# Kernel tuning notes

Hardware: AMD Instinct MI355X
Metric: run time of the kernel (lower is better)

Reference implementation:

```python
import jax, jax.numpy as jnp
import numpy as np

N = 100000   # nodes
E = 1000000  # edges
DIN = 128    # atom_in_features
DE = 16      # edge_attr_dim
H = 128      # hidden width (preprocess/cheb/postprocess)
K = 3        # Chebyshev order
EPS = 1e-5


def setup_inputs() -> dict:
    key = jax.random.key(0)
    ks = jax.random.split(key, 16)
    s = 0.02
    return {
        "x": jax.random.normal(ks[0], (N, DIN), jnp.float32),
        "edge_index": jax.random.randint(ks[1], (2, E), 0, N),
        "edge_attr": jax.random.normal(ks[2], (E, DE), jnp.float32),
        # AtomEdgeInteraction linear: (DIN+DE) -> H
        "w_int": jax.random.normal(ks[3], (DIN + DE, H), jnp.float32) * s,
        "b_int": jnp.zeros((H,), jnp.float32),
        # preprocess layer 1: Linear + BatchNorm + ReLU
        "w_pre": jax.random.normal(ks[4], (H, H), jnp.float32) * s,
        "b_pre": jnp.zeros((H,), jnp.float32),
        "g_pre": jnp.ones((H,), jnp.float32),
        "be_pre": jnp.zeros((H,), jnp.float32),
        # ChebConv layers: weight [K, in, out] + bias
        "cheb1_w": jax.random.normal(ks[5], (K, H, H), jnp.float32) * s,
        "cheb1_b": jnp.zeros((H,), jnp.float32),
        "cheb2_w": jax.random.normal(ks[6], (K, H, H), jnp.float32) * s,
        "cheb2_b": jnp.zeros((H,), jnp.float32),
        # postprocess: Linear + BatchNorm + ReLU
        "w_post": jax.random.normal(ks[7], (H, H), jnp.float32) * s,
        "b_post": jnp.zeros((H,), jnp.float32),
        "g_post": jnp.ones((H,), jnp.float32),
        "be_post": jnp.zeros((H,), jnp.float32),
        # output layer H -> 1
        "w_out": jax.random.normal(ks[8], (H, 1), jnp.float32) * s,
        "b_out": jnp.zeros((1,), jnp.float32),
    }


def _bn(z, g, b):
    # BatchNorm1d, training-mode batch statistics (biased variance, like torch)
    m = z.mean(0)
    v = ((z - m) ** 2).mean(0)
    return g * (z - m) * jax.lax.rsqrt(v + EPS) + b


def _cheb(h, W, b, row, col, norm):
    # ChebConv with sym normalization, lambda_max=2 => L_hat = -D^{-1/2} A D^{-1/2}
    def lhat(z):
        return jax.ops.segment_sum(norm[:, None] * z[row], col, num_segments=N)

    Tx0 = h
    out = Tx0 @ W[0]
    Tx1 = lhat(Tx0)
    out = out + Tx1 @ W[1]
    for k in range(2, W.shape[0]):
        Tx2 = 2.0 * lhat(Tx1) - Tx0
        out = out + Tx2 @ W[k]
        Tx0, Tx1 = Tx1, Tx2
    return out + b


def reference(x, edge_index, edge_attr,
              w_int, b_int,
              w_pre, b_pre, g_pre, be_pre,
              cheb1_w, cheb1_b, cheb2_w, cheb2_b,
              w_post, b_post, g_post, be_post,
              w_out, b_out):
    row, col = edge_index[0], edge_index[1]
    ones_e = jnp.ones((E,), x.dtype)

    # AtomEdgeInteraction: gather -> concat -> linear -> scatter_mean over col
    comb = jnp.concatenate([x[row], edge_attr], axis=-1)  # [E, DIN+DE]
    upd = comb @ w_int + b_int                             # [E, H]
    cnt = jax.ops.segment_sum(ones_e, col, num_segments=N)
    h = jax.ops.segment_sum(upd, col, num_segments=N) / jnp.clip(cnt, 1.0)[:, None]

    # preprocess layer 1 (Linear + BN + ReLU; dropout rate 0)
    h = jax.nn.relu(_bn(h @ w_pre + b_pre, g_pre, be_pre))

    # sym-normalized edge coefficients for scaled Laplacian
    deg = jax.ops.segment_sum(ones_e, row, num_segments=N)
    dis = jnp.where(deg > 0, jax.lax.rsqrt(jnp.maximum(deg, 1.0)), 0.0)
    norm = -dis[row] * dis[col]  # [E]

    h = jax.nn.relu(_cheb(h, cheb1_w, cheb1_b, row, col, norm))
    h = jax.nn.relu(_cheb(h, cheb2_w, cheb2_b, row, col, norm))

    # postprocess (Linear + BN + ReLU)
    h = jax.nn.relu(_bn(h @ w_post + b_post, g_post, be_post))

    # output layer, squeeze(-1) -> [N]
    return (h @ w_out + b_out).squeeze(-1)
```

## Files before the change

### kernel.cpp

```cpp
#include <hip/hip_runtime.h>
#include <hip/hip_bf16.h>

using u16 = unsigned short;
using u32 = unsigned int;

#define NN 100000
#define NE 1000000

typedef __attribute__((ext_vector_type(8))) short bfrag;
typedef __attribute__((ext_vector_type(4))) float ffrag;

__device__ __forceinline__ float bf2f(u16 u) { return __uint_as_float(((u32)u) << 16); }
__device__ __forceinline__ u16 f2bf(float f) {
  u32 x = __float_as_uint(f);
  return (u16)((x + 0x7fffu + ((x >> 16) & 1u)) >> 16);
}
__device__ __forceinline__ float rdv(const void* p, long i, int f) {
  return f ? bf2f(((const u16*)p)[i]) : ((const float*)p)[i];
}
__device__ __forceinline__ void acc8(float* a, uint4 v, float w) {
  a[0] = fmaf(w, __uint_as_float(v.x << 16), a[0]);
  a[1] = fmaf(w, __uint_as_float(v.x & 0xffff0000u), a[1]);
  a[2] = fmaf(w, __uint_as_float(v.y << 16), a[2]);
  a[3] = fmaf(w, __uint_as_float(v.y & 0xffff0000u), a[3]);
  a[4] = fmaf(w, __uint_as_float(v.z << 16), a[4]);
  a[5] = fmaf(w, __uint_as_float(v.z & 0xffff0000u), a[5]);
  a[6] = fmaf(w, __uint_as_float(v.w << 16), a[6]);
  a[7] = fmaf(w, __uint_as_float(v.w & 0xffff0000u), a[7]);
}

__global__ void k_flag(const u32* __restrict__ g_pre_raw, int* flag) {
  if (threadIdx.x == 0) flag[0] = (g_pre_raw[0] == 0x3F803F80u) ? 1 : 0;
}

#define OWXT 0
#define OWPRE 16384
#define OWD1 32768
#define OW11 49152
#define OV21 65536
#define OWD2 81920
#define OW12 98304
#define OV22 114688
#define OWPOST 131072
#define OWET 147456

struct PrepArgs { const void* in[16]; };

__global__ void k_prep(PrepArgs a, const int* __restrict__ flag, u16* __restrict__ wq,
                       float* __restrict__ wf) {
  int t = blockIdx.x * 256 + threadIdx.x;
  int f = *flag;
  if (t < 16384) {
    int o = t >> 7, k = t & 127;
    int ko = k * 128 + o;
    int ok = o * 128 + k;
    wq[OWXT + ok] = f2bf(rdv(a.in[0], ko, f));
    wq[OWPRE + ok] = f2bf(rdv(a.in[2], ko, f));
    float c0 = rdv(a.in[6], ko, f);
    float c1 = rdv(a.in[6], 16384 + ko, f);
    float c2 = rdv(a.in[6], 32768 + ko, f);
    wq[OWD1 + ok] = f2bf(c0 - c2);
    wq[OW11 + ok] = f2bf(c1);
    wq[OV21 + ok] = f2bf(2.f * c2);
    float d0 = rdv(a.in[8], ko, f);
    float d1 = rdv(a.in[8], 16384 + ko, f);
    float d2 = rdv(a.in[8], 32768 + ko, f);
    wq[OWD2 + ok] = f2bf(d0 - d2);
    wq[OW12 + ok] = f2bf(d1);
    wq[OV22 + ok] = f2bf(2.f * d2);
    wq[OWPOST + ok] = f2bf(rdv(a.in[10], ko, f));
  }
  if (t < 4096) {
    int o = t >> 5, k = t & 31;
    wq[OWET + o * 32 + k] = (k < 16) ? f2bf(rdv(a.in[0], (long)(128 + k) * 128 + o, f)) : (u16)0;
  }
  if (t < 1281) {
    int s = t >> 7, j = t & 127;
    const int map[11] = {1, 3, 4, 5, 7, 9, 11, 12, 13, 14, 15};
    wf[t] = rdv(a.in[map[s]], j, f);
  }
}

__global__ void k_hist(const int* __restrict__ ei, int* cnt, int* deg) {
  int e = blockIdx.x * 256 + threadIdx.x;
  if (e >= NE) return;
  atomicAdd(&deg[ei[e]], 1);
  atomicAdd(&cnt[ei[NE + e]], 1);
}

__global__ void k_scan1(const int* __restrict__ cnt, int* off, int* bsum) {
  __shared__ int s[1024];
  int t = threadIdx.x;
  int g = blockIdx.x * 1024 + t;
  int v = (g < NN) ? cnt[g] : 0;
  s[t] = v;
  __syncthreads();
  for (int st = 1; st < 1024; st <<= 1) {
    int x = (t >= st) ? s[t - st] : 0;
    __syncthreads();
    s[t] += x;
    __syncthreads();
  }
  if (g < NN) off[g] = s[t] - v;
  if (t == 1023) bsum[blockIdx.x] = s[t];
}

__global__ void k_scan2(int* bsum, int nb) {
  __shared__ int s[128];
  int t = threadIdx.x;
  int v = (t < nb) ? bsum[t] : 0;
  s[t] = v;
  __syncthreads();
  for (int st = 1; st < 128; st <<= 1) {
    int x = (t >= st) ? s[t - st] : 0;
    __syncthreads();
    s[t] += x;
    __syncthreads();
  }
  if (t < nb) bsum[t] = s[t] - v;
}

__global__ void k_scan3(int* off, const int* __restrict__ bsum,
                        const int* __restrict__ deg, float* __restrict__ dis) {
  int g = blockIdx.x * 1024 + threadIdx.x;
  if (g < NN) {
    off[g] += bsum[blockIdx.x];
    int d = deg[g];
    dis[g] = d > 0 ? rsqrtf((float)d) : 0.f;
  }
  if (g == 0) off[NN] = NE;
}

__global__ void k_place(const int* __restrict__ ei, const int* __restrict__ off,
                        int* cur, int* crow, int* ceid) {
  int e = blockIdx.x * 256 + threadIdx.x;
  if (e >= NE) return;
  int r = ei[e], c = ei[NE + e];
  int p = off[c] + atomicAdd(&cur[c], 1);
  crow[p] = r;
  ceid[p] = e;
}

__global__ __launch_bounds__(256) void k_spmm(const u16* __restrict__ src,
                                              u16* __restrict__ dst,
                                              const int* __restrict__ off,
                                              const int* __restrict__ crow,
                                              const float* __restrict__ dis,
                                              const u16* __restrict__ G, int relu) {
  int t = threadIdx.x;
  int node = blockIdx.x * 8 + (t >> 5);
  if (node >= NN) return;
  int l = t & 31;
  int half = l >> 4;
  int c = (l & 15) * 8;
  int p0 = off[node], p1 = off[node + 1];
  float a[8];
#pragma unroll
  for (int j = 0; j < 8; j++) a[j] = 0.f;
  const u16* sp = src + c;
  if (dis) {
    float nc = -dis[node];
    int p = p0 + half;
    for (; p + 6 < p1; p += 8) {
      int r0 = crow[p], r1 = crow[p + 2], r2 = crow[p + 4], r3 = crow[p + 6];
      float w0 = nc * dis[r0], w1 = nc * dis[r1];
      float w2 = nc * dis[r2], w3 = nc * dis[r3];
      uint4 v0 = *(const uint4*)(sp + (long)r0 * 128);
      uint4 v1 = *(const uint4*)(sp + (long)r1 * 128);
      uint4 v2 = *(const uint4*)(sp + (long)r2 * 128);
      uint4 v3 = *(const uint4*)(sp + (long)r3 * 128);
      acc8(a, v0, w0);
      acc8(a, v1, w1);
      acc8(a, v2, w2);
      acc8(a, v3, w3);
    }
    for (; p < p1; p += 2) {
      int r = crow[p];
      acc8(a, *(const uint4*)(sp + (long)r * 128), nc * dis[r]);
    }
  } else {
    int p = p0 + half;
    for (; p + 6 < p1; p += 8) {
      int r0 = crow[p], r1 = crow[p + 2], r2 = crow[p + 4], r3 = crow[p + 6];
      uint4 v0 = *(const uint4*)(sp + (long)r0 * 128);
      uint4 v1 = *(const uint4*)(sp + (long)r1 * 128);
      uint4 v2 = *(const uint4*)(sp + (long)r2 * 128);
      uint4 v3 = *(const uint4*)(sp + (long)r3 * 128);
      acc8(a, v0, 1.f);
      acc8(a, v1, 1.f);
      acc8(a, v2, 1.f);
      acc8(a, v3, 1.f);
    }
    for (; p < p1; p += 2) acc8(a, *(const uint4*)(sp + (long)crow[p] * 128), 1.f);
  }
#pragma unroll
  for (int j = 0; j < 8; j++) a[j] += __shfl_xor(a[j], 16);
  if (half) return;
  if (G) acc8(a, *(const uint4*)(G + (long)node * 128 + c), 1.f);
  if (relu) {
#pragma unroll
    for (int j = 0; j < 8; j++) a[j] = fmaxf(a[j], 0.f);
  }
  uint4 o;
  o.x = (u32)f2bf(a[0]) | ((u32)f2bf(a[1]) << 16);
  o.y = (u32)f2bf(a[2]) | ((u32)f2bf(a[3]) << 16);
  o.z = (u32)f2bf(a[4]) | ((u32)f2bf(a[5]) << 16);
  o.w = (u32)f2bf(a[6]) | ((u32)f2bf(a[7]) << 16);
  *(uint4*)(dst + (long)node * 128 + c) = o;
}

__global__ __launch_bounds__(256) void k_asum(const void* __restrict__ eattr,
                                              const int* __restrict__ flag,
                                              u16* __restrict__ asum,
                                              const int* __restrict__ off,
                                              const int* __restrict__ ceid) {
  int t = blockIdx.x * 256 + threadIdx.x;
  int node = t >> 4;
  if (node >= NN) return;
  int j = t & 15;
  int p0 = off[node], p1 = off[node + 1];
  float a = 0.f;
  if (*flag) {
    const u16* e16 = (const u16*)eattr;
    int p = p0;
    for (; p + 4 <= p1; p += 4) {
      float v0 = bf2f(e16[(long)ceid[p] * 16 + j]);
      float v1 = bf2f(e16[(long)ceid[p + 1] * 16 + j]);
      float v2 = bf2f(e16[(long)ceid[p + 2] * 16 + j]);
      float v3 = bf2f(e16[(long)ceid[p + 3] * 16 + j]);
      a += v0 + v1 + v2 + v3;
    }
    for (; p < p1; p++) a += bf2f(e16[(long)ceid[p] * 16 + j]);
  } else {
    const float* e32 = (const float*)eattr;
    int p = p0;
    for (; p + 4 <= p1; p += 4) {
      float v0 = e32[(long)ceid[p] * 16 + j];
      float v1 = e32[(long)ceid[p + 1] * 16 + j];
      float v2 = e32[(long)ceid[p + 2] * 16 + j];
      float v3 = e32[(long)ceid[p + 3] * 16 + j];
      a += v0 + v1 + v2 + v3;
    }
    for (; p < p1; p++) a += e32[(long)ceid[p] * 16 + j];
  }
  asum[(long)node * 32 + j] = f2bf(a);
  asum[(long)node * 32 + 16 + j] = 0;
}

struct MArgs {
  const void* A0; const u16* W0T; int a0raw;
  const u16* A1; const u16* W1T;
  const u16* W2T; u16* out2;
  const float* bias;
  const u16* G;
  u16* out;
  const int* cnt;
  const int* flag;
  float* part;
  int mode;
};

#define ASTRIDE 136
#define ESTRIDE 132

template <int DUAL, int K0>
__global__ __launch_bounds__(256) void k_mgemm(MArgs m) {
  __shared__ __align__(16) u16 sA[64 * ASTRIDE];
  int tid = threadIdx.x;
  int wv = tid >> 6, lane = tid & 63;
  int col16 = lane & 15, quad = lane >> 4;
  int r0 = blockIdx.x * 64;
  constexpr int NKB0 = K0 / 32;

  ffrag acc[8];
#pragma unroll
  for (int i = 0; i < 8; i++)
#pragma unroll
    for (int g = 0; g < 4; g++) acc[i][g] = 0.f;

  {
    int row = tid >> 2, seg = tid & 3;
    int ra = r0 + row;
    if (ra >= NN) ra = NN - 1;
    if (K0 == 128) {
      bool f32a = m.a0raw && (*m.flag == 0);
      if (f32a) {
        const float* gp = (const float*)m.A0 + (long)ra * 128 + seg * 32;
        u32* lp = (u32*)(sA + row * ASTRIDE + seg * 32);
#pragma unroll
        for (int e = 0; e < 4; e++) {
          float4 v0 = *(const float4*)(gp + e * 8);
          float4 v1 = *(const float4*)(gp + e * 8 + 4);
          lp[e * 4 + 0] = (u32)f2bf(v0.x) | ((u32)f2bf(v0.y) << 16);
          lp[e * 4 + 1] = (u32)f2bf(v0.z) | ((u32)f2bf(v0.w) << 16);
          lp[e * 4 + 2] = (u32)f2bf(v1.x) | ((u32)f2bf(v1.y) << 16);
          lp[e * 4 + 3] = (u32)f2bf(v1.z) | ((u32)f2bf(v1.w) << 16);
        }
      } else {
        const u16* gp = (const u16*)m.A0 + (long)ra * 128 + seg * 32;
        uint4* lp = (uint4*)(sA + row * ASTRIDE + seg * 32);
#pragma unroll
        for (int e = 0; e < 4; e++) lp[e] = *(const uint4*)(gp + e * 8);
      }
    } else {
      const u16* gp = (const u16*)m.A0 + (long)ra * 32 + seg * 8;
      *(uint4*)(sA + row * ASTRIDE + seg * 8) = *(const uint4*)gp;
    }
  }
  bfrag b0[2][NKB0];
#pragma unroll
  for (int c = 0; c < 2; c++)
#pragma unroll
    for (int kb = 0; kb < NKB0; kb++)
      b0[c][kb] = *(const bfrag*)(m.W0T + (long)(wv * 32 + c * 16 + col16) * K0 + kb * 32 + quad * 8);
  __syncthreads();
#pragma unroll
  for (int kb = 0; kb < NKB0; kb++)
#pragma unroll
    for (int rt = 0; rt < 4; rt++) {
      bfrag af = *(const bfrag*)(sA + (rt * 16 + col16) * ASTRIDE + kb * 32 + quad * 8);
      acc[rt * 2 + 0] = __builtin_amdgcn_mfma_f32_16x16x32_bf16(af, b0[0][kb], acc[rt * 2 + 0], 0, 0, 0);
      acc[rt * 2 + 1] = __builtin_amdgcn_mfma_f32_16x16x32_bf16(af, b0[1][kb], acc[rt * 2 + 1], 0, 0, 0);
    }

  ffrag acc2[DUAL ? 8 : 1];
  if constexpr (DUAL) {
#pragma unroll
    for (int i = 0; i < 8; i++)
#pragma unroll
      for (int g = 0; g < 4; g++) acc2[i][g] = 0.f;
    __syncthreads();
    {
      int row = tid >> 2, seg = tid & 3;
      int ra = r0 + row;
      if (ra >= NN) ra = NN - 1;
      const u16* gp = m.A1 + (long)ra * 128 + seg * 32;
      uint4* lp = (uint4*)(sA + row * ASTRIDE + seg * 32);
#pragma unroll
      for (int e = 0; e < 4; e++) lp[e] = *(const uint4*)(gp + e * 8);
    }
    bfrag b1[2][4], b2[2][4];
#pragma unroll
    for (int c = 0; c < 2; c++)
#pragma unroll
      for (int kb = 0; kb < 4; kb++) {
        b1[c][kb] = *(const bfrag*)(m.W1T + (long)(wv * 32 + c * 16 + col16) * 128 + kb * 32 + quad * 8);
        b2[c][kb] = *(const bfrag*)(m.W2T + (long)(wv * 32 + c * 16 + col16) * 128 + kb * 32 + quad * 8);
      }
    __syncthreads();
#pragma unroll
    for (int kb = 0; kb < 4; kb++)
#pragma unroll
      for (int rt = 0; rt < 4; rt++) {
        bfrag af = *(const bfrag*)(sA + (rt * 16 + col16) * ASTRIDE + kb * 32 + quad * 8);
        acc[rt * 2 + 0] = __builtin_amdgcn_mfma_f32_16x16x32_bf16(af, b1[0][kb], acc[rt * 2 + 0], 0, 0, 0);
        acc[rt * 2 + 1] = __builtin_amdgcn_mfma_f32_16x16x32_bf16(af, b1[1][kb], acc[rt * 2 + 1], 0, 0, 0);
        acc2[rt * 2 + 0] = __builtin_amdgcn_mfma_f32_16x16x32_bf16(af, b2[0][kb], acc2[rt * 2 + 0], 0, 0, 0);
        acc2[rt * 2 + 1] = __builtin_amdgcn_mfma_f32_16x16x32_bf16(af, b2[1][kb], acc2[rt * 2 + 1], 0, 0, 0);
      }
  }

  __syncthreads();
#pragma unroll
  for (int rt = 0; rt < 4; rt++)
#pragma unroll
    for (int c = 0; c < 2; c++) {
      int col = wv * 32 + c * 16 + col16;
      float bj = m.bias ? m.bias[col] : 0.f;
#pragma unroll
      for (int g = 0; g < 4; g++) {
        int r = r0 + rt * 16 + quad * 4 + g;
        float v = acc[rt * 2 + c][g];
        if (m.G && r < NN) v += bf2f(m.G[(long)r * 128 + col]);
        if (m.mode == 2) {
          int cc = (r < NN) ? m.cnt[r] : 0;
          v = (v + (float)cc * bj) / (float)(cc > 1 ? cc : 1);
        } else {
          v += bj;
        }
        sA[(rt * 16 + quad * 4 + g) * ESTRIDE + col] = f2bf(v);
      }
    }
  __syncthreads();
  {
    int rr = tid >> 2, d = tid & 3;
    int row = r0 + rr;
    if (row < NN) {
      const uint2* s2 = (const uint2*)(sA + rr * ESTRIDE + d * 32);
      uint2 a0 = s2[0], a1 = s2[1], a2 = s2[2], a3 = s2[3];
      uint2 a4 = s2[4], a5 = s2[5], a6 = s2[6], a7 = s2[7];
      uint4* o = (uint4*)(m.out + (long)row * 128 + d * 32);
      o[0] = make_uint4(a0.x, a0.y, a1.x, a1.y);
      o[1] = make_uint4(a2.x, a2.y, a3.x, a3.y);
      o[2] = make_uint4(a4.x, a4.y, a5.x, a5.y);
      o[3] = make_uint4(a6.x, a6.y, a7.x, a7.y);
    }
  }
  if (m.part) {
    __shared__ float ps[256], pq[256];
    int col = tid & 127, hf = tid >> 7;
    float s = 0.f, q = 0.f;
#pragma unroll
    for (int r = 0; r < 32; r++) {
      int rr = hf * 32 + r;
      if (r0 + rr < NN) {
        float v = bf2f(sA[rr * ESTRIDE + col]);
        s += v;
        q += v * v;
      }
    }
    ps[tid] = s;
    pq[tid] = q;
    __syncthreads();
    if (tid < 128) {
      m.part[(long)blockIdx.x * 256 + tid] = ps[tid] + ps[tid + 128];
      m.part[(long)blockIdx.x * 256 + 128 + tid] = pq[tid] + pq[tid + 128];
    }
  }
  if constexpr (DUAL) {
    __syncthreads();
#pragma unroll
    for (int rt = 0; rt < 4; rt++)
#pragma unroll
      for (int c = 0; c < 2; c++) {
        int col = wv * 32 + c * 16 + col16;
#pragma unroll
        for (int g = 0; g < 4; g++)
          sA[(rt * 16 + quad * 4 + g) * ESTRIDE + col] = f2bf(acc2[rt * 2 + c][g]);
      }
    __syncthreads();
    int rr = tid >> 2, d = tid & 3;
    int row = r0 + rr;
    if (row < NN) {
      const uint2* s2 = (const uint2*)(sA + rr * ESTRIDE + d * 32);
      uint2 a0 = s2[0], a1 = s2[1], a2 = s2[2], a3 = s2[3];
      uint2 a4 = s2[4], a5 = s2[5], a6 = s2[6], a7 = s2[7];
      uint4* o = (uint4*)(m.out2 + (long)row * 128 + d * 32);
      o[0] = make_uint4(a0.x, a0.y, a1.x, a1.y);
      o[1] = make_uint4(a2.x, a2.y, a3.x, a3.y);
      o[2] = make_uint4(a4.x, a4.y, a5.x, a5.y);
      o[3] = make_uint4(a6.x, a6.y, a7.x, a7.y);
    }
  }
}

__global__ void k_red(const float* __restrict__ part, float* stats, int nblk) {
  int j = threadIdx.x;
  float s = 0.f;
  for (int b = blockIdx.x; b < nblk; b += gridDim.x) s += part[(long)b * 256 + j];
  atomicAdd(&stats[j], s);
}

__global__ void k_bnfin(const float* __restrict__ stats, const float* __restrict__ gamma,
                        const float* __restrict__ beta, float* ab) {
  int j = threadIdx.x;
  if (j >= 128) return;
  float m = stats[j] * (1.f / (float)NN);
  float v = fmaxf(stats[128 + j] * (1.f / (float)NN) - m * m, 0.f);
  float a = gamma[j] * rsqrtf(v + 1e-5f);
  float c = beta[j] - m * a;
  ab[j] = a;
  ab[128 + j] = c;
}

__global__ void k_bnrelu(const u16* __restrict__ z, u16* __restrict__ out,
                         const float* __restrict__ ab) {
  long idx = (long)blockIdx.x * 256 + threadIdx.x;
  long t = idx * 2;
  if (t >= (long)NN * 128) return;
  int col = (int)(t & 127);
  u32 v = *(const u32*)(z + t);
  float f0 = fmaxf(__uint_as_float(v << 16) * ab[col] + ab[128 + col], 0.f);
  float f1 = fmaxf(__uint_as_float(v & 0xffff0000u) * ab[col + 1] + ab[129 + col], 0.f);
  *(u32*)(out + t) = (u32)f2bf(f0) | ((u32)f2bf(f1) << 16);
}

__global__ void k_out(const u16* __restrict__ z, const float* __restrict__ ab,
                      const float* __restrict__ wout, const float* __restrict__ bout,
                      const int* __restrict__ flag, void* __restrict__ y) {
  int node = blockIdx.x * 4 + (threadIdx.x >> 6);
  if (node >= NN) return;
  int lane = threadIdx.x & 63;
  float s = 0.f;
#pragma unroll
  for (int c = lane; c < 128; c += 64) {
    float zz = bf2f(z[(long)node * 128 + c]);
    float h = fmaxf(ab[c] * zz + ab[128 + c], 0.f);
    s += h * wout[c];
  }
#pragma unroll
  for (int o = 32; o > 0; o >>= 1) s += __shfl_down(s, o);
  if (lane == 0) {
    float r = s + bout[0];
    if (*flag) ((u16*)y)[node] = f2bf(r);
    else ((float*)y)[node] = r;
  }
}

extern "C" void kernel_launch(void* const* d_in, const int* in_sizes, int n_in,
                              void* d_out, int out_size, void* d_ws, size_t ws_size,
                              hipStream_t stream) {
  const void* x = d_in[0];
  const int* ei = (const int*)d_in[1];
  const void* eattr = d_in[2];
  (void)in_sizes; (void)n_in; (void)out_size; (void)ws_size;

  char* w = (char*)d_ws;
  size_t p = 0;
  auto alloc = [&](size_t b) { size_t r = p; p += (b + 255) & ~(size_t)255; return r; };
  size_t o_cnt = alloc((size_t)NN * 4);
  size_t o_deg = alloc((size_t)NN * 4);
  size_t o_cur = alloc((size_t)NN * 4);
  size_t o_zero_end = p;
  size_t o_dis = alloc((size_t)NN * 4);
  size_t o_off = alloc((size_t)(NN + 1) * 4);
  size_t o_bsum = alloc(1024 * 4);
  size_t o_stat = alloc(512 * 4);
  size_t o_ab = alloc(512 * 4);
  size_t o_flag = alloc(256);
  size_t o_wq = alloc((size_t)151552 * 2);
  size_t o_wf = alloc((size_t)1281 * 4);
  size_t o_crow = alloc((size_t)NE * 4);
  size_t o_asum = alloc((size_t)NN * 32 * 2);
  size_t o_part = alloc((size_t)1563 * 256 * 4);
  size_t o_Bx = alloc((size_t)NN * 128 * 2);
  size_t o_Bt = alloc((size_t)NN * 128 * 2);

  int* cnt = (int*)(w + o_cnt);
  int* deg = (int*)(w + o_deg);
  int* cur = (int*)(w + o_cur);
  float* dis = (float*)(w + o_dis);
  int* off = (int*)(w + o_off);
  int* bsum = (int*)(w + o_bsum);
  float* statA = (float*)(w + o_stat);
  float* statB = statA + 256;
  float* abA = (float*)(w + o_ab);
  float* abB = abA + 256;
  int* flag = (int*)(w + o_flag);
  u16* wq = (u16*)(w + o_wq);
  float* wf = (float*)(w + o_wf);
  int* crow = (int*)(w + o_crow);
  u16* asum = (u16*)(w + o_asum);
  float* part = (float*)(w + o_part);
  u16* Bx = (u16*)(w + o_Bx);
  u16* Bt = (u16*)(w + o_Bt);
  int* ceid = (int*)Bt;

  hipMemsetAsync(w + o_cnt, 0, o_zero_end - o_cnt, stream);
  hipMemsetAsync(w + o_stat, 0, 512 * 4, stream);

  int gE = (NE + 255) / 256;
  int nb = (NN + 1023) / 1024;
  int gS = (NN + 7) / 8;
  int gG = (NN + 63) / 64;

  k_flag<<<1, 64, 0, stream>>>((const u32*)d_in[7], flag);
  {
    PrepArgs a;
    for (int i = 0; i < 16; i++) a.in[i] = d_in[3 + i];
    k_prep<<<64, 256, 0, stream>>>(a, flag, wq, wf);
  }

  k_hist<<<gE, 256, 0, stream>>>(ei, cnt, deg);
  k_scan1<<<nb, 1024, 0, stream>>>(cnt, off, bsum);
  k_scan2<<<1, 128, 0, stream>>>(bsum, nb);
  k_scan3<<<nb, 1024, 0, stream>>>(off, bsum, deg, dis);
  k_place<<<gE, 256, 0, stream>>>(ei, off, cur, crow, ceid);
  k_asum<<<(NN * 16 + 255) / 256, 256, 0, stream>>>(eattr, flag, asum, off, ceid);

  {
    MArgs a = {};
    a.A0 = x; a.W0T = wq + OWXT; a.a0raw = 1;
    a.out = Bx; a.flag = flag; a.mode = 0;
    k_mgemm<0, 128><<<gG, 256, 0, stream>>>(a);
  }
  k_spmm<<<gS, 256, 0, stream>>>(Bx, Bt, off, crow, nullptr, nullptr, 0);
  {
    MArgs a = {};
    a.A0 = asum; a.W0T = wq + OWET;
    a.bias = wf + 0; a.G = Bt; a.out = Bx; a.cnt = cnt; a.flag = flag; a.mode = 2;
    k_mgemm<0, 32><<<gG, 256, 0, stream>>>(a);
  }

  {
    MArgs a = {};
    a.A0 = Bx; a.W0T = wq + OWPRE;
    a.bias = wf + 128; a.out = Bt; a.flag = flag; a.part = part; a.mode = 0;
    k_mgemm<0, 128><<<gG, 256, 0, stream>>>(a);
  }
  k_red<<<32, 256, 0, stream>>>(part, statA, gG);
  k_bnfin<<<1, 128, 0, stream>>>(statA, wf + 256, wf + 384, abA);
  k_bnrelu<<<(int)(((long)NN * 128 / 2 + 255) / 256), 256, 0, stream>>>(Bt, Bx, abA);

  k_spmm<<<gS, 256, 0, stream>>>(Bx, Bt, off, crow, dis, nullptr, 0);
  {
    MArgs a = {};
    a.A0 = Bx; a.W0T = wq + OWD1;
    a.A1 = Bt; a.W1T = wq + OW11;
    a.W2T = wq + OV21; a.out2 = Bt;
    a.bias = wf + 512; a.out = Bx; a.flag = flag; a.mode = 0;
    k_mgemm<1, 128><<<gG, 256, 0, stream>>>(a);
  }
  k_spmm<<<gS, 256, 0, stream>>>(Bt, Bx, off, crow, dis, Bx, 1);

  k_spmm<<<gS, 256, 0, stream>>>(Bx, Bt, off, crow, dis, nullptr, 0);
  {
    MArgs a = {};
    a.A0 = Bx; a.W0T = wq + OWD2;
    a.A1 = Bt; a.W1T = wq + OW12;
    a.W2T = wq + OV22; a.out2 = Bt;
    a.bias = wf + 640; a.out = Bx; a.flag = flag; a.mode = 0;
    k_mgemm<1, 128><<<gG, 256, 0, stream>>>(a);
  }
  k_spmm<<<gS, 256, 0, stream>>>(Bt, Bx, off, crow, dis, Bx, 1);

  {
    MArgs a = {};
    a.A0 = Bx; a.W0T = wq + OWPOST;
    a.bias = wf + 768; a.out = Bt; a.flag = flag; a.part = part; a.mode = 0;
    k_mgemm<0, 128><<<gG, 256, 0, stream>>>(a);
  }
  k_red<<<32, 256, 0, stream>>>(part, statB, gG);
  k_bnfin<<<1, 128, 0, stream>>>(statB, wf + 896, wf + 1024, abB);
  k_out<<<(NN + 3) / 4, 256, 0, stream>>>(Bt, abB, wf + 1152, wf + 1280, flag, d_out);
}
```

Baseline: 806.6 us.

## Fuse histogram with first GEMM, drop flag/scan kernels, enlarge GEMM tiles

Runs the edge histogram inside the same launch as the first node GEMM, so the atomic histogram work overlaps the x·W GEMM. Each edge now records its atomic rank, which replaces the second atomic pass in the CSR placement. The scan2/scan3 kernels, the flag kernel and a memset are merged or removed. Several GEMMs move to 128-row tiles with fewer blocks, and the BN partial reduction is rewritten to write stats deterministically without atomics. These changes cut launch overhead and atomics, at the cost of fewer GEMM blocks and more register pressure per block.

```diff
diff --git a/kernel.cpp b/kernel.cpp
--- a/kernel.cpp
+++ b/kernel.cpp
@@ -9,6 +9,8 @@
 
 typedef __attribute__((ext_vector_type(8))) short bfrag;
 typedef __attribute__((ext_vector_type(4))) float ffrag;
+
+#define BF16ONE2 0x3F803F80u
 
 __device__ __forceinline__ float bf2f(u16 u) { return __uint_as_float(((u32)u) << 16); }
 __device__ __forceinline__ u16 f2bf(float f) {
@@ -27,10 +29,6 @@
   a[5] = fmaf(w, __uint_as_float(v.z & 0xffff0000u), a[5]);
   a[6] = fmaf(w, __uint_as_float(v.w << 16), a[6]);
   a[7] = fmaf(w, __uint_as_float(v.w & 0xffff0000u), a[7]);
-}
-
-__global__ void k_flag(const u32* __restrict__ g_pre_raw, int* flag) {
-  if (threadIdx.x == 0) flag[0] = (g_pre_raw[0] == 0x3F803F80u) ? 1 : 0;
 }
 
 #define OWXT 0
@@ -46,10 +44,10 @@
 
 struct PrepArgs { const void* in[16]; };
 
-__global__ void k_prep(PrepArgs a, const int* __restrict__ flag, u16* __restrict__ wq,
+__global__ void k_prep(PrepArgs a, const u32* __restrict__ gp, u16* __restrict__ wq,
                        float* __restrict__ wf) {
   int t = blockIdx.x * 256 + threadIdx.x;
-  int f = *flag;
+  int f = (gp[0] == BF16ONE2) ? 1 : 0;
   if (t < 16384) {
     int o = t >> 7, k = t & 127;
     int ko = k * 128 + o;
@@ -81,13 +79,6 @@
   }
 }
 
-__global__ void k_hist(const int* __restrict__ ei, int* cnt, int* deg) {
-  int e = blockIdx.x * 256 + threadIdx.x;
-  if (e >= NE) return;
-  atomicAdd(&deg[ei[e]], 1);
-  atomicAdd(&cnt[ei[NE + e]], 1);
-}
-
 __global__ void k_scan1(const int* __restrict__ cnt, int* off, int* bsum) {
   __shared__ int s[1024];
   int t = threadIdx.x;
@@ -105,26 +96,28 @@
   if (t == 1023) bsum[blockIdx.x] = s[t];
 }
 
-__global__ void k_scan2(int* bsum, int nb) {
+__global__ void k_scan23(int* off, const int* __restrict__ bsum,
+                         const int* __restrict__ deg, float* __restrict__ dis, int nb) {
   __shared__ int s[128];
   int t = threadIdx.x;
-  int v = (t < nb) ? bsum[t] : 0;
-  s[t] = v;
+  int v = 0;
+  if (t < 128) {
+    v = (t < nb) ? bsum[t] : 0;
+    s[t] = v;
+  }
   __syncthreads();
   for (int st = 1; st < 128; st <<= 1) {
-    int x = (t >= st) ? s[t - st] : 0;
-    __syncthreads();
-    s[t] += x;
-    __syncthreads();
-  }
-  if (t < nb) bsum[t] = s[t] - v;
-}
-
-__global__ void k_scan3(int* off, const int* __restrict__ bsum,
-                        const int* __restrict__ deg, float* __restrict__ dis) {
-  int g = blockIdx.x * 1024 + threadIdx.x;
+    int x = (t >= st && t < 128) ? s[t - st] : 0;
+    __syncthreads();
+    if (t < 128) s[t] += x;
+    __syncthreads();
+  }
+  if (t < 128) s[t] -= v;
+  __syncthreads();
+  int pre = s[blockIdx.x];
+  int g = blockIdx.x * 1024 + t;
   if (g < NN) {
-    off[g] += bsum[blockIdx.x];
+    off[g] += pre;
     int d = deg[g];
     dis[g] = d > 0 ? rsqrtf((float)d) : 0.f;
   }
@@ -132,11 +125,11 @@
 }
 
 __global__ void k_place(const int* __restrict__ ei, const int* __restrict__ off,
-                        int* cur, int* crow, int* ceid) {
+                        const int* __restrict__ rank, int* crow, int* ceid) {
   int e = blockIdx.x * 256 + threadIdx.x;
   if (e >= NE) return;
   int r = ei[e], c = ei[NE + e];
-  int p = off[c] + atomicAdd(&cur[c], 1);
+  int p = off[c] + rank[e];
   crow[p] = r;
   ceid[p] = e;
 }
@@ -210,7 +203,7 @@
 }
 
 __global__ __launch_bounds__(256) void k_asum(const void* __restrict__ eattr,
-                                              const int* __restrict__ flag,
+                                              const u32* __restrict__ gp,
                                               u16* __restrict__ asum,
                                               const int* __restrict__ off,
                                               const int* __restrict__ ceid) {
@@ -220,7 +213,7 @@
   int j = t & 15;
   int p0 = off[node], p1 = off[node + 1];
   float a = 0.f;
-  if (*flag) {
+  if (gp[0] == BF16ONE2) {
     const u16* e16 = (const u16*)eattr;
     int p = p0;
     for (; p + 4 <= p1; p += 4) {
@@ -255,7 +248,7 @@
   const u16* G;
   u16* out;
   const int* cnt;
-  const int* flag;
+  const u32* gp;
   float* part;
   int mode;
 };
@@ -263,48 +256,46 @@
 #define ASTRIDE 136
 #define ESTRIDE 132
 
-template <int DUAL, int K0>
-__global__ __launch_bounds__(256) void k_mgemm(MArgs m) {
-  __shared__ __align__(16) u16 sA[64 * ASTRIDE];
+template <int DUAL, int K0, int ROWS>
+__device__ __forceinline__ void mgemm_body(const MArgs& m, int blk) {
+  constexpr int RT = ROWS / 16;
+  constexpr int TPR = 256 / ROWS;
+  constexpr int SEGW = K0 / TPR;
+  constexpr int NKB0 = K0 / 32;
+  __shared__ __align__(16) u16 sA[ROWS * ASTRIDE];
   int tid = threadIdx.x;
   int wv = tid >> 6, lane = tid & 63;
   int col16 = lane & 15, quad = lane >> 4;
-  int r0 = blockIdx.x * 64;
-  constexpr int NKB0 = K0 / 32;
-
-  ffrag acc[8];
-#pragma unroll
-  for (int i = 0; i < 8; i++)
+  int r0 = blk * ROWS;
+
+  ffrag acc[RT * 2];
+#pragma unroll
+  for (int i = 0; i < RT * 2; i++)
 #pragma unroll
     for (int g = 0; g < 4; g++) acc[i][g] = 0.f;
 
   {
-    int row = tid >> 2, seg = tid & 3;
+    int row = tid / TPR, seg = tid % TPR;
     int ra = r0 + row;
     if (ra >= NN) ra = NN - 1;
-    if (K0 == 128) {
-      bool f32a = m.a0raw && (*m.flag == 0);
-      if (f32a) {
-        const float* gp = (const float*)m.A0 + (long)ra * 128 + seg * 32;
-        u32* lp = (u32*)(sA + row * ASTRIDE + seg * 32);
-#pragma unroll
-        for (int e = 0; e < 4; e++) {
-          float4 v0 = *(const float4*)(gp + e * 8);
-          float4 v1 = *(const float4*)(gp + e * 8 + 4);
-          lp[e * 4 + 0] = (u32)f2bf(v0.x) | ((u32)f2bf(v0.y) << 16);
-          lp[e * 4 + 1] = (u32)f2bf(v0.z) | ((u32)f2bf(v0.w) << 16);
-          lp[e * 4 + 2] = (u32)f2bf(v1.x) | ((u32)f2bf(v1.y) << 16);
-          lp[e * 4 + 3] = (u32)f2bf(v1.z) | ((u32)f2bf(v1.w) << 16);
-        }
-      } else {
-        const u16* gp = (const u16*)m.A0 + (long)ra * 128 + seg * 32;
-        uint4* lp = (uint4*)(sA + row * ASTRIDE + seg * 32);
-#pragma unroll
-        for (int e = 0; e < 4; e++) lp[e] = *(const uint4*)(gp + e * 8);
+    bool f32a = m.a0raw && (m.gp[0] != BF16ONE2);
+    if (f32a) {
+      const float* gs = (const float*)m.A0 + (long)ra * K0 + seg * SEGW;
+      u32* lp = (u32*)(sA + row * ASTRIDE + seg * SEGW);
+#pragma unroll
+      for (int e = 0; e < SEGW / 8; e++) {
+        float4 v0 = *(const float4*)(gs + e * 8);
+        float4 v1 = *(const float4*)(gs + e * 8 + 4);
+        lp[e * 4 + 0] = (u32)f2bf(v0.x) | ((u32)f2bf(v0.y) << 16);
+        lp[e * 4 + 1] = (u32)f2bf(v0.z) | ((u32)f2bf(v0.w) << 16);
+        lp[e * 4 + 2] = (u32)f2bf(v1.x) | ((u32)f2bf(v1.y) << 16);
+        lp[e * 4 + 3] = (u32)f2bf(v1.z) | ((u32)f2bf(v1.w) << 16);
       }
     } else {
-      const u16* gp = (const u16*)m.A0 + (long)ra * 32 + seg * 8;
-      *(uint4*)(sA + row * ASTRIDE + seg * 8) = *(const uint4*)gp;
+      const u16* gs = (const u16*)m.A0 + (long)ra * K0 + seg * SEGW;
+      uint4* lp = (uint4*)(sA + row * ASTRIDE + seg * SEGW);
+#pragma unroll
+      for (int e = 0; e < SEGW / 8; e++) lp[e] = *(const uint4*)(gs + e * 8);
     }
   }
   bfrag b0[2][NKB0];
@@ -317,27 +308,27 @@
 #pragma unroll
   for (int kb = 0; kb < NKB0; kb++)
 #pragma unroll
-    for (int rt = 0; rt < 4; rt++) {
+    for (int rt = 0; rt < RT; rt++) {
       bfrag af = *(const bfrag*)(sA + (rt * 16 + col16) * ASTRIDE + kb * 32 + quad * 8);
       acc[rt * 2 + 0] = __builtin_amdgcn_mfma_f32_16x16x32_bf16(af, b0[0][kb], acc[rt * 2 + 0], 0, 0, 0);
       acc[rt * 2 + 1] = __builtin_amdgcn_mfma_f32_16x16x32_bf16(af, b0[1][kb], acc[rt * 2 + 1], 0, 0, 0);
     }
 
-  ffrag acc2[DUAL ? 8 : 1];
+  ffrag acc2[DUAL ? RT * 2 : 1];
   if constexpr (DUAL) {
 #pragma unroll
-    for (int i = 0; i < 8; i++)
+    for (int i = 0; i < RT * 2; i++)
 #pragma unroll
       for (int g = 0; g < 4; g++) acc2[i][g] = 0.f;
     __syncthreads();
     {
-      int row = tid >> 2, seg = tid & 3;
+      int row = tid / TPR, seg = tid % TPR;
       int ra = r0 + row;
       if (ra >= NN) ra = NN - 1;
-      const u16* gp = m.A1 + (long)ra * 128 + seg * 32;
-      uint4* lp = (uint4*)(sA + row * ASTRIDE + seg * 32);
-#pragma unroll
-      for (int e = 0; e < 4; e++) lp[e] = *(const uint4*)(gp + e * 8);
+      const u16* gs = m.A1 + (long)ra * 128 + seg * SEGW;
+      uint4* lp = (uint4*)(sA + row * ASTRIDE + seg * SEGW);
+#pragma unroll
+      for (int e = 0; e < SEGW / 8; e++) lp[e] = *(const uint4*)(gs + e * 8);
     }
     bfrag b1[2][4], b2[2][4];
 #pragma unroll
@@ -351,7 +342,7 @@
 #pragma unroll
     for (int kb = 0; kb < 4; kb++)
 #pragma unroll
-      for (int rt = 0; rt < 4; rt++) {
+      for (int rt = 0; rt < RT; rt++) {
         bfrag af = *(const bfrag*)(sA + (rt * 16 + col16) * ASTRIDE + kb * 32 + quad * 8);
         acc[rt * 2 + 0] = __builtin_amdgcn_mfma_f32_16x16x32_bf16(af, b1[0][kb], acc[rt * 2 + 0], 0, 0, 0);
         acc[rt * 2 + 1] = __builtin_amdgcn_mfma_f32_16x16x32_bf16(af, b1[1][kb], acc[rt * 2 + 1], 0, 0, 0);
@@ -362,7 +353,7 @@
 
   __syncthreads();
 #pragma unroll
-  for (int rt = 0; rt < 4; rt++)
+  for (int rt = 0; rt < RT; rt++)
 #pragma unroll
     for (int c = 0; c < 2; c++) {
       int col = wv * 32 + c * 16 + col16;
@@ -383,17 +374,18 @@
     }
   __syncthreads();
   {
-    int rr = tid >> 2, d = tid & 3;
-    int row = r0 + rr;
-    if (row < NN) {
-      const uint2* s2 = (const uint2*)(sA + rr * ESTRIDE + d * 32);
-      uint2 a0 = s2[0], a1 = s2[1], a2 = s2[2], a3 = s2[3];
-      uint2 a4 = s2[4], a5 = s2[5], a6 = s2[6], a7 = s2[7];
-      uint4* o = (uint4*)(m.out + (long)row * 128 + d * 32);
-      o[0] = make_uint4(a0.x, a0.y, a1.x, a1.y);
-      o[1] = make_uint4(a2.x, a2.y, a3.x, a3.y);
-      o[2] = make_uint4(a4.x, a4.y, a5.x, a5.y);
-      o[3] = make_uint4(a6.x, a6.y, a7.x, a7.y);
+    constexpr int CPT = 128 / TPR;
+    int rr = tid / TPR, d = tid % TPR;
+    int rowg = r0 + rr;
+    if (rowg < NN) {
+      const u16* sp2 = sA + rr * ESTRIDE + d * CPT;
+      uint4* o = (uint4*)(m.out + (long)rowg * 128 + d * CPT);
+#pragma unroll
+      for (int e = 0; e < CPT / 8; e++) {
+        const uint2* s2 = (const uint2*)(sp2 + e * 8);
+        uint2 lo = s2[0], hi = s2[1];
+        o[e] = make_uint4(lo.x, lo.y, hi.x, hi.y);
+      }
     }
   }
   if (m.part) {
@@ -401,8 +393,8 @@
     int col = tid & 127, hf = tid >> 7;
     float s = 0.f, q = 0.f;
 #pragma unroll
-    for (int r = 0; r < 32; r++) {
-      int rr = hf * 32 + r;
+    for (int r = 0; r < ROWS / 2; r++) {
+      int rr = hf * (ROWS / 2) + r;
       if (r0 + rr < NN) {
         float v = bf2f(sA[rr * ESTRIDE + col]);
         s += v;
@@ -413,14 +405,14 @@
     pq[tid] = q;
     __syncthreads();
     if (tid < 128) {
-      m.part[(long)blockIdx.x * 256 + tid] = ps[tid] + ps[tid + 128];
-      m.part[(long)blockIdx.x * 256 + 128 + tid] = pq[tid] + pq[tid + 128];
+      m.part[(long)blk * 256 + tid] = ps[tid] + ps[tid + 128];
+      m.part[(long)blk * 256 + 128 + tid] = pq[tid] + pq[tid + 128];
     }
   }
   if constexpr (DUAL) {
     __syncthreads();
 #pragma unroll
-    for (int rt = 0; rt < 4; rt++)
+    for (int rt = 0; rt < RT; rt++)
 #pragma unroll
       for (int c = 0; c < 2; c++) {
         int col = wv * 32 + c * 16 + col16;
@@ -429,26 +421,58 @@
           sA[(rt * 16 + quad * 4 + g) * ESTRIDE + col] = f2bf(acc2[rt * 2 + c][g]);
       }
     __syncthreads();
-    int rr = tid >> 2, d = tid & 3;
-    int row = r0 + rr;
-    if (row < NN) {
-      const uint2* s2 = (const uint2*)(sA + rr * ESTRIDE + d * 32);
-      uint2 a0 = s2[0], a1 = s2[1], a2 = s2[2], a3 = s2[3];
-      uint2 a4 = s2[4], a5 = s2[5], a6 = s2[6], a7 = s2[7];
-      uint4* o = (uint4*)(m.out2 + (long)row * 128 + d * 32);
-      o[0] = make_uint4(a0.x, a0.y, a1.x, a1.y);
-      o[1] = make_uint4(a2.x, a2.y, a3.x, a3.y);
-      o[2] = make_uint4(a4.x, a4.y, a5.x, a5.y);
-      o[3] = make_uint4(a6.x, a6.y, a7.x, a7.y);
-    }
+    constexpr int CPT = 128 / TPR;
+    int rr = tid / TPR, d = tid % TPR;
+    int rowg = r0 + rr;
+    if (rowg < NN) {
+      const u16* sp2 = sA + rr * ESTRIDE + d * CPT;
+      uint4* o = (uint4*)(m.out2 + (long)rowg * 128 + d * CPT);
+#pragma unroll
+      for (int e = 0; e < CPT / 8; e++) {
+        const uint2* s2 = (const uint2*)(sp2 + e * 8);
+        uint2 lo = s2[0], hi = s2[1];
+        o[e] = make_uint4(lo.x, lo.y, hi.x, hi.y);
+      }
+    }
+  }
+}
+
+template <int DUAL, int K0, int ROWS>
+__global__ __launch_bounds__(256) void k_mgemm(MArgs m) {
+  mgemm_body<DUAL, K0, ROWS>(m, blockIdx.x);
+}
+
+__global__ __launch_bounds__(256) void k_mega(MArgs m, int gemmBlocks,
+                                              const int* __restrict__ ei, int* cnt,
+                                              int* deg, int* rank, int histBlocks) {
+  if ((int)blockIdx.x < gemmBlocks) {
+    mgemm_body<0, 128, 128>(m, blockIdx.x);
+    return;
+  }
+  int hb = blockIdx.x - gemmBlocks;
+  int stride = histBlocks * 256;
+  for (int e = hb * 256 + (int)threadIdx.x; e < NE; e += stride) {
+    int r = ei[e], c = ei[NE + e];
+    rank[e] = atomicAdd(&cnt[c], 1);
+    atomicAdd(&deg[r], 1);
   }
 }
 
 __global__ void k_red(const float* __restrict__ part, float* stats, int nblk) {
-  int j = threadIdx.x;
+  int tid = threadIdx.x;
+  int j = blockIdx.x * 32 + (tid & 31);
+  int ch = tid >> 5;
   float s = 0.f;
-  for (int b = blockIdx.x; b < nblk; b += gridDim.x) s += part[(long)b * 256 + j];
-  atomicAdd(&stats[j], s);
+  for (int b = ch; b < nblk; b += 8) s += part[(long)b * 256 + j];
+  __shared__ float sh[256];
+  sh[tid] = s;
+  __syncthreads();
+  if (tid < 32) {
+    float t = 0.f;
+#pragma unroll
+    for (int i = 0; i < 8; i++) t += sh[i * 32 + tid];
+    stats[blockIdx.x * 32 + tid] = t;
+  }
 }
 
 __global__ void k_bnfin(const float* __restrict__ stats, const float* __restrict__ gamma,
@@ -477,7 +501,7 @@
 
 __global__ void k_out(const u16* __restrict__ z, const float* __restrict__ ab,
                       const float* __restrict__ wout, const float* __restrict__ bout,
-                      const int* __restrict__ flag, void* __restrict__ y) {
+                      const u32* __restrict__ gp, void* __restrict__ y) {
   int node = blockIdx.x * 4 + (threadIdx.x >> 6);
   if (node >= NN) return;
   int lane = threadIdx.x & 63;
@@ -492,7 +516,7 @@
   for (int o = 32; o > 0; o >>= 1) s += __shfl_down(s, o);
   if (lane == 0) {
     float r = s + bout[0];
-    if (*flag) ((u16*)y)[node] = f2bf(r);
+    if (gp[0] == BF16ONE2) ((u16*)y)[node] = f2bf(r);
     else ((float*)y)[node] = r;
   }
 }
@@ -503,6 +527,7 @@
   const void* x = d_in[0];
   const int* ei = (const int*)d_in[1];
   const void* eattr = d_in[2];
+  const u32* gp = (const u32*)d_in[7];
   (void)in_sizes; (void)n_in; (void)out_size; (void)ws_size;
 
   char* w = (char*)d_ws;
@@ -510,25 +535,22 @@
   auto alloc = [&](size_t b) { size_t r = p; p += (b + 255) & ~(size_t)255; return r; };
   size_t o_cnt = alloc((size_t)NN * 4);
   size_t o_deg = alloc((size_t)NN * 4);
-  size_t o_cur = alloc((size_t)NN * 4);
   size_t o_zero_end = p;
   size_t o_dis = alloc((size_t)NN * 4);
   size_t o_off = alloc((size_t)(NN + 1) * 4);
   size_t o_bsum = alloc(1024 * 4);
   size_t o_stat = alloc(512 * 4);
   size_t o_ab = alloc(512 * 4);
-  size_t o_flag = alloc(256);
   size_t o_wq = alloc((size_t)151552 * 2);
   size_t o_wf = alloc((size_t)1281 * 4);
   size_t o_crow = alloc((size_t)NE * 4);
   size_t o_asum = alloc((size_t)NN * 32 * 2);
-  size_t o_part = alloc((size_t)1563 * 256 * 4);
+  size_t o_part = alloc((size_t)782 * 256 * 4);
   size_t o_Bx = alloc((size_t)NN * 128 * 2);
   size_t o_Bt = alloc((size_t)NN * 128 * 2);
 
   int* cnt = (int*)(w + o_cnt);
   int* deg = (int*)(w + o_deg);
-  int* cur = (int*)(w + o_cur);
   float* dis = (float*)(w + o_dis);
   int* off = (int*)(w + o_off);
   int* bsum = (int*)(w + o_bsum);
@@ -536,7 +558,6 @@
   float* statB = statA + 256;
   float* abA = (float*)(w + o_ab);
   float* abB = abA + 256;
-  int* flag = (int*)(w + o_flag);
   u16* wq = (u16*)(w + o_wq);
   float* wf = (float*)(w + o_wf);
   int* crow = (int*)(w + o_crow);
@@ -544,51 +565,50 @@
   float* part = (float*)(w + o_part);
   u16* Bx = (u16*)(w + o_Bx);
   u16* Bt = (u16*)(w + o_Bt);
+  int* rank = (int*)asum;
   int* ceid = (int*)Bt;
 
   hipMemsetAsync(w + o_cnt, 0, o_zero_end - o_cnt, stream);
-  hipMemsetAsync(w + o_stat, 0, 512 * 4, stream);
 
   int gE = (NE + 255) / 256;
   int nb = (NN + 1023) / 1024;
   int gS = (NN + 7) / 8;
-  int gG = (NN + 63) / 64;
-
-  k_flag<<<1, 64, 0, stream>>>((const u32*)d_in[7], flag);
+  int gG1 = (NN + 127) / 128;
+  int gG2 = (NN + 63) / 64;
+  int histB = 1024;
+
   {
     PrepArgs a;
     for (int i = 0; i < 16; i++) a.in[i] = d_in[3 + i];
-    k_prep<<<64, 256, 0, stream>>>(a, flag, wq, wf);
-  }
-
-  k_hist<<<gE, 256, 0, stream>>>(ei, cnt, deg);
-  k_scan1<<<nb, 1024, 0, stream>>>(cnt, off, bsum);
-  k_scan2<<<1, 128, 0, stream>>>(bsum, nb);
-  k_scan3<<<nb, 1024, 0, stream>>>(off, bsum, deg, dis);
-  k_place<<<gE, 256, 0, stream>>>(ei, off, cur, crow, ceid);
-  k_asum<<<(NN * 16 + 255) / 256, 256, 0, stream>>>(eattr, flag, asum, off, ceid);
+    k_prep<<<64, 256, 0, stream>>>(a, gp, wq, wf);
+  }
 
   {
     MArgs a = {};
     a.A0 = x; a.W0T = wq + OWXT; a.a0raw = 1;
-    a.out = Bx; a.flag = flag; a.mode = 0;
-    k_mgemm<0, 128><<<gG, 256, 0, stream>>>(a);
-  }
+    a.out = Bx; a.gp = gp; a.mode = 0;
+    k_mega<<<gG1 + histB, 256, 0, stream>>>(a, gG1, ei, cnt, deg, rank, histB);
+  }
+  k_scan1<<<nb, 1024, 0, stream>>>(cnt, off, bsum);
+  k_scan23<<<nb, 1024, 0, stream>>>(off, bsum, deg, dis, nb);
+  k_place<<<gE, 256, 0, stream>>>(ei, off, rank, crow, ceid);
+  k_asum<<<(NN * 16 + 255) / 256, 256, 0, stream>>>(eattr, gp, asum, off, ceid);
+
   k_spmm<<<gS, 256, 0, stream>>>(Bx, Bt, off, crow, nullptr, nullptr, 0);
   {
     MArgs a = {};
     a.A0 = asum; a.W0T = wq + OWET;
-    a.bias = wf + 0; a.G = Bt; a.out = Bx; a.cnt = cnt; a.flag = flag; a.mode = 2;
-    k_mgemm<0, 32><<<gG, 256, 0, stream>>>(a);
+    a.bias = wf + 0; a.G = Bt; a.out = Bx; a.cnt = cnt; a.gp = gp; a.mode = 2;
+    k_mgemm<0, 32, 128><<<gG1, 256, 0, stream>>>(a);
   }
 
   {
     MArgs a = {};
     a.A0 = Bx; a.W0T = wq + OWPRE;
-    a.bias = wf + 128; a.out = Bt; a.flag = flag; a.part = part; a.mode = 0;
-    k_mgemm<0, 128><<<gG, 256, 0, stream>>>(a);
-  }
-  k_red<<<32, 256, 0, stream>>>(part, statA, gG);
+    a.bias = wf + 128; a.out = Bt; a.gp = gp; a.part = part; a.mode = 0;
+    k_mgemm<0, 128, 128><<<gG1, 256, 0, stream>>>(a);
+  }
+  k_red<<<8, 256, 0, stream>>>(part, statA, gG1);
   k_bnfin<<<1, 128, 0, stream>>>(statA, wf + 256, wf + 384, abA);
   k_bnrelu<<<(int)(((long)NN * 128 / 2 + 255) / 256), 256, 0, stream>>>(Bt, Bx, abA);
 
@@ -598,8 +618,8 @@
     a.A0 = Bx; a.W0T = wq + OWD1;
     a.A1 = Bt; a.W1T = wq + OW11;
     a.W2T = wq + OV21; a.out2 = Bt;
-    a.bias = wf + 512; a.out = Bx; a.flag = flag; a.mode = 0;
-    k_mgemm<1, 128><<<gG, 256, 0, stream>>>(a);
+    a.bias = wf + 512; a.out = Bx; a.gp = gp; a.mode = 0;
+    k_mgemm<1, 128, 64><<<gG2, 256, 0, stream>>>(a);
   }
   k_spmm<<<gS, 256, 0, stream>>>(Bt, Bx, off, crow, dis, Bx, 1);
 
@@ -609,18 +629,18 @@
     a.A0 = Bx; a.W0T = wq + OWD2;
     a.A1 = Bt; a.W1T = wq + OW12;
     a.W2T = wq + OV22; a.out2 = Bt;
-    a.bias = wf + 640; a.out = Bx; a.flag = flag; a.mode = 0;
-    k_mgemm<1, 128><<<gG, 256, 0, stream>>>(a);
+    a.bias = wf + 640; a.out = Bx; a.gp = gp; a.mode = 0;
+    k_mgemm<1, 128, 64><<<gG2, 256, 0, stream>>>(a);
   }
   k_spmm<<<gS, 256, 0, stream>>>(Bt, Bx, off, crow, dis, Bx, 1);
 
   {
     MArgs a = {};
     a.A0 = Bx; a.W0T = wq + OWPOST;
-    a.bias = wf + 768; a.out = Bt; a.flag = flag; a.part = part; a.mode = 0;
-    k_mgemm<0, 128><<<gG, 256, 0, stream>>>(a);
-  }
-  k_red<<<32, 256, 0, stream>>>(part, statB, gG);
+    a.bias = wf + 768; a.out = Bt; a.gp = gp; a.part = part; a.mode = 0;
+    k_mgemm<0, 128, 128><<<gG1, 256, 0, stream>>>(a);
+  }
+  k_red<<<8, 256, 0, stream>>>(part, statB, gG1);
   k_bnfin<<<1, 128, 0, stream>>>(statB, wf + 896, wf + 1024, abB);
-  k_out<<<(NN + 3) / 4, 256, 0, stream>>>(Bt, abB, wf + 1152, wf + 1280, flag, d_out);
-}
+  k_out<<<(NN + 3) / 4, 256, 0, stream>>>(Bt, abB, wf + 1152, wf + 1280, gp, d_out);
+}
```

After: 853.7 us. +5.8%, slower.
